# Kernel tuning notes

Measured on AMD Instinct MI355X. Metric: run time of the kernel, lower is better.

The kernel has to match this reference:

```python
import jax, jax.numpy as jnp
import numpy as np

N_NODES = 50000
N_EDGES = 800000
IN_CH = 256
HID = 256
NUM_GRAPHS = 512
LEAKY_SLOPE = 0.01
EPS = 1e-5


def gcn_conv(x, src, dst, W, b):
    # src/dst already include self loops. Symmetric normalization D^-1/2 A_hat D^-1/2.
    deg = jnp.zeros((N_NODES,), x.dtype).at[dst].add(1.0)
    dinv = jax.lax.rsqrt(deg)  # deg >= 1 because of self loops
    norm = dinv[src] * dinv[dst]  # [E+N]
    h = x @ W  # [N, H] dense GEMM
    agg = jnp.zeros((N_NODES, W.shape[1]), x.dtype).at[dst].add(h[src] * norm[:, None])
    return agg + b


def layer_norm(x, w, b):
    mu = jnp.mean(x, axis=-1, keepdims=True)
    var = jnp.mean(jnp.square(x - mu), axis=-1, keepdims=True)
    return (x - mu) * jax.lax.rsqrt(var + EPS) * w + b


def setup_inputs() -> dict:
    key = jax.random.key(0)
    ks = jax.random.split(key, 8)
    x = jax.random.normal(ks[0], (N_NODES, IN_CH), dtype=jnp.float32)
    edge_index = jax.random.randint(ks[1], (2, N_EDGES), 0, N_NODES, dtype=jnp.int64)
    batch = jnp.sort(jax.random.randint(ks[2], (N_NODES,), 0, NUM_GRAPHS, dtype=jnp.int64))
    s1 = (2.0 / IN_CH) ** 0.5
    s2 = (2.0 / HID) ** 0.5
    W1 = jax.random.normal(ks[3], (IN_CH, HID), dtype=jnp.float32) * s1
    b1 = jnp.zeros((HID,), jnp.float32)
    W2 = jax.random.normal(ks[4], (HID, HID), dtype=jnp.float32) * s2
    b2 = jnp.zeros((HID,), jnp.float32)
    ln1_w = jnp.ones((HID,), jnp.float32)
    ln1_b = jnp.zeros((HID,), jnp.float32)
    ln2_w = jnp.ones((HID,), jnp.float32)
    ln2_b = jnp.zeros((HID,), jnp.float32)
    return {"x": x, "edge_index": edge_index, "batch": batch,
            "W1": W1, "b1": b1, "ln1_w": ln1_w, "ln1_b": ln1_b,
            "W2": W2, "b2": b2, "ln2_w": ln2_w, "ln2_b": ln2_b}


def reference(x, edge_index, batch, W1, b1, ln1_w, ln1_b, W2, b2, ln2_w, ln2_b):
    loop = jnp.arange(N_NODES, dtype=edge_index.dtype)
    src = jnp.concatenate([edge_index[0], loop])
    dst = jnp.concatenate([edge_index[1], loop])

    h = gcn_conv(x, src, dst, W1, b1)
    h = layer_norm(h, ln1_w, ln1_b)
    h = jnp.where(h >= 0, h, LEAKY_SLOPE * h)

    h = gcn_conv(h, src, dst, W2, b2)
    h = layer_norm(h, ln2_w, ln2_b)
    h = jnp.where(h >= 0, h, LEAKY_SLOPE * h)

    # global mean pool per graph (dropout is inference no-op)
    sums = jax.ops.segment_sum(h, batch, num_segments=NUM_GRAPHS)
    cnts = jax.ops.segment_sum(jnp.ones((N_NODES,), h.dtype), batch, num_segments=NUM_GRAPHS)
    return sums / jnp.maximum(cnts, 1.0)[:, None]
```

## Files before the change

kernel.cpp:

```cpp
#include <hip/hip_runtime.h>

#define N_NODES 50000
#define N_EDGES 800000
#define CH 256
#define NUM_GRAPHS 512
#define LEAKY 0.01f
#define LN_EPS 1e-5f
#define NBLK ((N_NODES + 255) / 256)

typedef __attribute__((ext_vector_type(4))) float f32x4;
typedef __attribute__((ext_vector_type(2))) float f32x2;
typedef __attribute__((ext_vector_type(8))) short bf16x8;

__device__ __forceinline__ float b2f(unsigned short u) {
    union { unsigned int i; float f; } x; x.i = ((unsigned int)u) << 16; return x.f;
}
__device__ __forceinline__ unsigned short f2b(float f) {
    union { float f; unsigned int i; } x; x.f = f;
    unsigned int r = x.i + 0x7fffu + ((x.i >> 16) & 1u);
    return (unsigned short)(r >> 16);
}
__device__ __forceinline__ f32x2 b2f2(unsigned int u) {
    union { unsigned int i; float f; } lo, hi;
    lo.i = u << 16; hi.i = u & 0xffff0000u;
    f32x2 r; r.x = lo.f; r.y = hi.f; return r;
}
__device__ __forceinline__ unsigned int pack2(float a, float b) {
    return (unsigned int)f2b(a) | ((unsigned int)f2b(b) << 16);
}
__device__ __forceinline__ void gload16(const void* g, void* l) {
    __builtin_amdgcn_global_load_lds((const __attribute__((address_space(1))) unsigned int*)g,
                                     (__attribute__((address_space(3))) unsigned int*)l, 16, 0, 0);
}

__global__ void zero_ints(int* __restrict__ p, int n) {
    int i = blockIdx.x * blockDim.x + threadIdx.x;
    if (i < n) p[i] = 0;
}

__global__ void count_deg(const int* __restrict__ dst, int* __restrict__ cnt) {
    int e = blockIdx.x * blockDim.x + threadIdx.x;
    if (e < N_EDGES) atomicAdd(&cnt[dst[e]], 1);
}

__global__ __launch_bounds__(256) void block_reduce(const int* __restrict__ cnt,
                                                    int* __restrict__ bsum,
                                                    float* __restrict__ dinv) {
    __shared__ int s[256];
    int tid = threadIdx.x;
    int i = blockIdx.x * 256 + tid;
    int v = (i < N_NODES) ? cnt[i] : 0;
    if (i < N_NODES) dinv[i] = rsqrtf(1.0f + (float)v);
    s[tid] = v;
    __syncthreads();
    #pragma unroll
    for (int off = 128; off > 0; off >>= 1) {
        if (tid < off) s[tid] += s[tid + off];
        __syncthreads();
    }
    if (tid == 0) bsum[blockIdx.x] = s[0];
}

__global__ __launch_bounds__(256) void scan_bsums(int* __restrict__ bsum) {
    __shared__ int s[256];
    int tid = threadIdx.x;
    int v = (tid < NBLK) ? bsum[tid] : 0;
    s[tid] = v;
    __syncthreads();
    #pragma unroll
    for (int off = 1; off < 256; off <<= 1) {
        int t = (tid >= off) ? s[tid - off] : 0;
        __syncthreads();
        s[tid] += t;
        __syncthreads();
    }
    if (tid < NBLK) bsum[tid] = s[tid] - v;
}

__global__ __launch_bounds__(256) void block_scan(const int* __restrict__ cnt,
                                                  const int* __restrict__ bsum,
                                                  int* __restrict__ rowptr,
                                                  int* __restrict__ cursor) {
    __shared__ int s[256];
    int tid = threadIdx.x;
    int i = blockIdx.x * 256 + tid;
    int v = (i < N_NODES) ? cnt[i] : 0;
    s[tid] = v;
    __syncthreads();
    #pragma unroll
    for (int off = 1; off < 256; off <<= 1) {
        int t = (tid >= off) ? s[tid - off] : 0;
        __syncthreads();
        s[tid] += t;
        __syncthreads();
    }
    if (i < N_NODES) {
        int val = bsum[blockIdx.x] + s[tid] - v;
        rowptr[i] = val;
        cursor[i] = val;
        if (i == N_NODES - 1) rowptr[N_NODES] = bsum[blockIdx.x] + s[tid];
    }
}

__global__ void fill_csr(const int* __restrict__ src, const int* __restrict__ dst,
                         int* __restrict__ cursor, int* __restrict__ col) {
    int e = blockIdx.x * blockDim.x + threadIdx.x;
    if (e < N_EDGES) {
        int d = dst[e];
        int p = atomicAdd(&cursor[d], 1);
        col[p] = src[e];
    }
}

__global__ void transpose_w2(const float* __restrict__ W1f, const float* __restrict__ W2f,
                             unsigned short* __restrict__ WT1, unsigned short* __restrict__ WT2) {
    int k = blockIdx.x & 255;
    const float* W = (blockIdx.x >> 8) ? W2f : W1f;
    unsigned short* WT = (blockIdx.x >> 8) ? WT2 : WT1;
    int n = threadIdx.x;
    WT[n * CH + k] = f2b(W[k * CH + n]);
}

#define BM 128
#define BN 128
#define BK 64
#define SWZ(row, kb) (((row) * 128 + (kb) * 16) ^ (((row) & 7) << 4))

__global__ __launch_bounds__(256) void gemm_bf16(const unsigned short* __restrict__ A,
                                                 const unsigned short* __restrict__ BT,
                                                 const float* __restrict__ dinv,
                                                 unsigned short* __restrict__ out) {
    __shared__ unsigned short As[BM * BK];
    __shared__ unsigned short Bs[BN * BK];
    const int row0 = blockIdx.x * BM;
    const int col0 = blockIdx.y * BN;
    const int tid = threadIdx.x;
    const int w = tid >> 6, l = tid & 63;
    const int wr = w >> 1, wc = w & 1;
    const int lr = l & 15, lg = l >> 4;

    const int sr = l >> 3;
    const int kbp = l & 7;

    f32x4 acc[4][4] = {};

    for (int k0 = 0; k0 < CH; k0 += BK) {
        #pragma unroll
        for (int it = 0; it < 4; it++) {
            const int R = (w * 4 + it) * 8;
            const int r = R + sr;
            const int kb = kbp ^ (r & 7);
            gload16(&A[(size_t)(row0 + r) * CH + k0 + kb * 8], (char*)As + R * 128);
            gload16(&BT[(size_t)(col0 + r) * CH + k0 + kb * 8], (char*)Bs + R * 128);
        }
        __syncthreads();
        #pragma unroll
        for (int ks = 0; ks < 2; ks++) {
            bf16x8 af[4], bfr[4];
            #pragma unroll
            for (int fm = 0; fm < 4; fm++) {
                int r = wr * 64 + fm * 16 + lr;
                af[fm] = *(const bf16x8*)((const char*)As + SWZ(r, ks * 4 + lg));
            }
            #pragma unroll
            for (int fn = 0; fn < 4; fn++) {
                int r = wc * 64 + fn * 16 + lr;
                bfr[fn] = *(const bf16x8*)((const char*)Bs + SWZ(r, ks * 4 + lg));
            }
            #pragma unroll
            for (int fm = 0; fm < 4; fm++)
                #pragma unroll
                for (int fn = 0; fn < 4; fn++)
                    acc[fm][fn] = __builtin_amdgcn_mfma_f32_16x16x32_bf16(af[fm], bfr[fn], acc[fm][fn], 0, 0, 0);
        }
        __syncthreads();
    }
    #pragma unroll
    for (int fm = 0; fm < 4; fm++) {
        #pragma unroll
        for (int r = 0; r < 4; r++) {
            int grow = row0 + wr * 64 + fm * 16 + lg * 4 + r;
            if (grow < N_NODES) {
                float s = dinv[grow];
                #pragma unroll
                for (int fn = 0; fn < 4; fn++) {
                    int gcol = col0 + wc * 64 + fn * 16 + lr;
                    out[(size_t)grow * CH + gcol] = f2b(acc[fm][fn][r] * s);
                }
            }
        }
    }
}

__global__ __launch_bounds__(256) void gemm_f32a(const float* __restrict__ Af,
                                                 const unsigned short* __restrict__ BT,
                                                 const float* __restrict__ dinv,
                                                 unsigned short* __restrict__ out) {
    __shared__ unsigned short As[BM * BK];
    __shared__ unsigned short Bs[BN * BK];
    const int row0 = blockIdx.x * BM;
    const int col0 = blockIdx.y * BN;
    const int tid = threadIdx.x;
    const int w = tid >> 6, l = tid & 63;
    const int wr = w >> 1, wc = w & 1;
    const int lr = l & 15, lg = l >> 4;
    const int sr = l >> 3, kbp = l & 7;

    f32x4 acc[4][4] = {};

    for (int k0 = 0; k0 < CH; k0 += BK) {
        #pragma unroll
        for (int it = 0; it < 4; it++) {
            const int R = (w * 4 + it) * 8;
            const int r = R + sr;
            const int kb = kbp ^ (r & 7);
            gload16(&BT[(size_t)(col0 + r) * CH + k0 + kb * 8], (char*)Bs + R * 128);
        }
        #pragma unroll
        for (int it = 0; it < 4; it++) {
            int cidx = it * 256 + tid;
            int r = cidx >> 3, kb = cidx & 7;
            int grow = row0 + r;
            uint4 ua = make_uint4(0u, 0u, 0u, 0u);
            if (grow < N_NODES) {
                const float* ap = &Af[(size_t)grow * CH + k0 + kb * 8];
                float4 v0 = *(const float4*)ap;
                float4 v1 = *(const float4*)(ap + 4);
                ua = make_uint4(pack2(v0.x, v0.y), pack2(v0.z, v0.w),
                                pack2(v1.x, v1.y), pack2(v1.z, v1.w));
            }
            *(uint4*)((char*)As + SWZ(r, kb)) = ua;
        }
        __syncthreads();
        #pragma unroll
        for (int ks = 0; ks < 2; ks++) {
            bf16x8 af[4], bfr[4];
            #pragma unroll
            for (int fm = 0; fm < 4; fm++) {
                int r = wr * 64 + fm * 16 + lr;
                af[fm] = *(const bf16x8*)((const char*)As + SWZ(r, ks * 4 + lg));
            }
            #pragma unroll
            for (int fn = 0; fn < 4; fn++) {
                int r = wc * 64 + fn * 16 + lr;
                bfr[fn] = *(const bf16x8*)((const char*)Bs + SWZ(r, ks * 4 + lg));
            }
            #pragma unroll
            for (int fm = 0; fm < 4; fm++)
                #pragma unroll
                for (int fn = 0; fn < 4; fn++)
                    acc[fm][fn] = __builtin_amdgcn_mfma_f32_16x16x32_bf16(af[fm], bfr[fn], acc[fm][fn], 0, 0, 0);
        }
        __syncthreads();
    }
    #pragma unroll
    for (int fm = 0; fm < 4; fm++) {
        #pragma unroll
        for (int r = 0; r < 4; r++) {
            int grow = row0 + wr * 64 + fm * 16 + lg * 4 + r;
            if (grow < N_NODES) {
                float s = dinv[grow];
                #pragma unroll
                for (int fn = 0; fn < 4; fn++) {
                    int gcol = col0 + wc * 64 + fn * 16 + lr;
                    out[(size_t)grow * CH + gcol] = f2b(acc[fm][fn][r] * s);
                }
            }
        }
    }
}

__global__ __launch_bounds__(256) void agg_ln_bf16(const unsigned short* __restrict__ h,
                                                   const int* __restrict__ rowptr,
                                                   const int* __restrict__ col,
                                                   const float* __restrict__ dinv,
                                                   const float* __restrict__ bias,
                                                   const float* __restrict__ lnw,
                                                   const float* __restrict__ lnb,
                                                   unsigned short* __restrict__ out) {
    const int w = threadIdx.x >> 6, lane = threadIdx.x & 63;
    const int d = blockIdx.x * 4 + w;
    if (d >= N_NODES) return;
    const int c4 = lane * 4;
    const uint2* __restrict__ h2 = (const uint2*)h;

    f32x2 acc01, acc23;
    {
        uint2 u = h2[(unsigned)(d * 64 + lane)];
        acc01 = b2f2(u.x); acc23 = b2f2(u.y);
    }

    const int e0 = rowptr[d], e1 = rowptr[d + 1];
    for (int base = e0; base < e1; base += 64) {
        int nch = e1 - base; if (nch > 64) nch = 64;
        int cidx = (lane < nch) ? col[base + lane] : 0;
        int j = 0;
        for (; j + 8 <= nch; j += 8) {
            int s0 = __shfl(cidx, j),     s1 = __shfl(cidx, j + 1);
            int s2 = __shfl(cidx, j + 2), s3 = __shfl(cidx, j + 3);
            int s4 = __shfl(cidx, j + 4), s5 = __shfl(cidx, j + 5);
            int s6 = __shfl(cidx, j + 6), s7 = __shfl(cidx, j + 7);
            uint2 u0 = h2[(unsigned)(s0 * 64 + lane)];
            uint2 u1 = h2[(unsigned)(s1 * 64 + lane)];
            uint2 u2 = h2[(unsigned)(s2 * 64 + lane)];
            uint2 u3 = h2[(unsigned)(s3 * 64 + lane)];
            uint2 u4 = h2[(unsigned)(s4 * 64 + lane)];
            uint2 u5 = h2[(unsigned)(s5 * 64 + lane)];
            uint2 u6 = h2[(unsigned)(s6 * 64 + lane)];
            uint2 u7 = h2[(unsigned)(s7 * 64 + lane)];
            acc01 += b2f2(u0.x) + b2f2(u1.x) + b2f2(u2.x) + b2f2(u3.x);
            acc23 += b2f2(u0.y) + b2f2(u1.y) + b2f2(u2.y) + b2f2(u3.y);
            acc01 += b2f2(u4.x) + b2f2(u5.x) + b2f2(u6.x) + b2f2(u7.x);
            acc23 += b2f2(u4.y) + b2f2(u5.y) + b2f2(u6.y) + b2f2(u7.y);
        }
        for (; j + 4 <= nch; j += 4) {
            int s0 = __shfl(cidx, j),     s1 = __shfl(cidx, j + 1);
            int s2 = __shfl(cidx, j + 2), s3 = __shfl(cidx, j + 3);
            uint2 u0 = h2[(unsigned)(s0 * 64 + lane)];
            uint2 u1 = h2[(unsigned)(s1 * 64 + lane)];
            uint2 u2 = h2[(unsigned)(s2 * 64 + lane)];
            uint2 u3 = h2[(unsigned)(s3 * 64 + lane)];
            acc01 += b2f2(u0.x) + b2f2(u1.x) + b2f2(u2.x) + b2f2(u3.x);
            acc23 += b2f2(u0.y) + b2f2(u1.y) + b2f2(u2.y) + b2f2(u3.y);
        }
        for (; j < nch; j++) {
            int s = __shfl(cidx, j);
            uint2 u = h2[(unsigned)(s * 64 + lane)];
            acc01 += b2f2(u.x); acc23 += b2f2(u.y);
        }
    }
    float a0 = acc01.x, a1 = acc01.y, a2 = acc23.x, a3 = acc23.y;
    const float di = dinv[d];
    float4 bb = *(const float4*)&bias[c4];
    a0 = a0 * di + bb.x; a1 = a1 * di + bb.y; a2 = a2 * di + bb.z; a3 = a3 * di + bb.w;

    float s1 = a0 + a1 + a2 + a3;
    float s2 = a0 * a0 + a1 * a1 + a2 * a2 + a3 * a3;
    #pragma unroll
    for (int off = 32; off > 0; off >>= 1) {
        s1 += __shfl_xor(s1, off);
        s2 += __shfl_xor(s2, off);
    }
    const float mu = s1 * (1.0f / CH);
    const float rstd = rsqrtf(s2 * (1.0f / CH) - mu * mu + LN_EPS);
    float4 wv = *(const float4*)&lnw[c4];
    float4 bv = *(const float4*)&lnb[c4];
    float y0 = (a0 - mu) * rstd * wv.x + bv.x;
    float y1 = (a1 - mu) * rstd * wv.y + bv.y;
    float y2 = (a2 - mu) * rstd * wv.z + bv.z;
    float y3 = (a3 - mu) * rstd * wv.w + bv.w;
    y0 = (y0 >= 0.f) ? y0 : LEAKY * y0;
    y1 = (y1 >= 0.f) ? y1 : LEAKY * y1;
    y2 = (y2 >= 0.f) ? y2 : LEAKY * y2;
    y3 = (y3 >= 0.f) ? y3 : LEAKY * y3;
    *(ushort4*)&out[(size_t)d * CH + c4] = make_ushort4(f2b(y0), f2b(y1), f2b(y2), f2b(y3));
}

__global__ __launch_bounds__(256) void pool_mean_bf16(const unsigned short* __restrict__ feat,
                                                      const int* __restrict__ batch,
                                                      float* __restrict__ out) {
    const int g = blockIdx.x;
    const int w = threadIdx.x >> 6, lane = threadIdx.x & 63;
    int lo = 0, hi = N_NODES;
    while (lo < hi) { int mid = (lo + hi) >> 1; if (batch[mid] < g) lo = mid + 1; else hi = mid; }
    const int start = lo;
    hi = N_NODES;
    while (lo < hi) { int mid = (lo + hi) >> 1; if (batch[mid] < g + 1) lo = mid + 1; else hi = mid; }
    const int end = lo;

    float a0 = 0.f, a1 = 0.f, a2 = 0.f, a3 = 0.f;
    for (int n = start + w; n < end; n += 4) {
        ushort4 u = *(const ushort4*)&feat[(size_t)n * CH + lane * 4];
        a0 += b2f(u.x); a1 += b2f(u.y); a2 += b2f(u.z); a3 += b2f(u.w);
    }
    __shared__ float4 red[4][64];
    red[w][lane] = make_float4(a0, a1, a2, a3);
    __syncthreads();
    if (w == 0) {
        float4 t0 = red[0][lane], t1 = red[1][lane], t2 = red[2][lane], t3 = red[3][lane];
        const float inv = (end > start) ? 1.0f / (float)(end - start) : 0.0f;
        float4 o = make_float4((t0.x + t1.x + t2.x + t3.x) * inv,
                               (t0.y + t1.y + t2.y + t3.y) * inv,
                               (t0.z + t1.z + t2.z + t3.z) * inv,
                               (t0.w + t1.w + t2.w + t3.w) * inv);
        *(float4*)&out[(size_t)g * CH + lane * 4] = o;
    }
}

static inline size_t align256(size_t x) { return (x + 255) & ~(size_t)255; }

extern "C" void kernel_launch(void* const* d_in, const int* in_sizes, int n_in,
                              void* d_out, int out_size, void* d_ws, size_t ws_size,
                              hipStream_t stream) {
    const float* x    = (const float*)d_in[0];
    const int*   edge = (const int*)d_in[1];
    const int*   batch= (const int*)d_in[2];
    const float* W1   = (const float*)d_in[3];
    const float* b1   = (const float*)d_in[4];
    const float* ln1w = (const float*)d_in[5];
    const float* ln1b = (const float*)d_in[6];
    const float* W2   = (const float*)d_in[7];
    const float* b2   = (const float*)d_in[8];
    const float* ln2w = (const float*)d_in[9];
    const float* ln2b = (const float*)d_in[10];

    const int* src = edge;
    const int* dst = edge + N_EDGES;

    char* p = (char*)d_ws;
    int* cnt    = (int*)p;  p += align256(N_NODES * 4);
    int* cursor = (int*)p;  p += align256(N_NODES * 4);
    int* rowptr = (int*)p;  p += align256((N_NODES + 1) * 4);
    int* bsum   = (int*)p;  p += align256(NBLK * 4);
    float* dinv = (float*)p; p += align256(N_NODES * 4);
    int* col    = (int*)p;  p += align256(N_EDGES * 4);
    unsigned short* wt1 = (unsigned short*)p; p += align256(CH * CH * 2);
    unsigned short* wt2 = (unsigned short*)p; p += align256(CH * CH * 2);
    unsigned short* bufA = (unsigned short*)p; p += align256((size_t)N_NODES * CH * 2);
    unsigned short* bufB = (unsigned short*)p; p += align256((size_t)N_NODES * CH * 2);
    p += 32768;

    zero_ints<<<(N_NODES + 255) / 256, 256, 0, stream>>>(cnt, N_NODES);
    count_deg<<<(N_EDGES + 255) / 256, 256, 0, stream>>>(dst, cnt);
    block_reduce<<<NBLK, 256, 0, stream>>>(cnt, bsum, dinv);
    scan_bsums<<<1, 256, 0, stream>>>(bsum);
    block_scan<<<NBLK, 256, 0, stream>>>(cnt, bsum, rowptr, cursor);
    fill_csr<<<(N_EDGES + 255) / 256, 256, 0, stream>>>(src, dst, cursor, col);
    transpose_w2<<<2 * CH, CH, 0, stream>>>(W1, W2, wt1, wt2);

    dim3 ggrid((N_NODES + BM - 1) / BM, CH / BN);
    gemm_f32a<<<ggrid, 256, 0, stream>>>(x, wt1, dinv, bufA);
    agg_ln_bf16<<<(N_NODES + 3) / 4, 256, 0, stream>>>(bufA, rowptr, col, dinv, b1, ln1w, ln1b, bufB);
    gemm_bf16<<<ggrid, 256, 0, stream>>>(bufB, wt2, dinv, bufA);
    agg_ln_bf16<<<(N_NODES + 3) / 4, 256, 0, stream>>>(bufA, rowptr, col, dinv, b2, ln2w, ln2b, bufB);
    pool_mean_bf16<<<NUM_GRAPHS, 256, 0, stream>>>(bufB, batch, (float*)d_out);
}
```

Measured before the change: 293.0 us.

## Widen GEMM tiles to full width and fuse small setup kernels

Each GEMM block now covers all 256 output columns (BN=256) instead of 128, so every A tile is loaded into LDS only once. This cuts A-side global traffic and halves the grid, at the cost of twice the accumulator registers and more LDS per block, which may lower occupancy. The count-zeroing and weight-transpose kernels are merged into one launch, and the block-sum scan is folded into block_scan so each block redoes it redundantly. LeakyReLU becomes a single fmaxf.

```diff
diff --git a/kernel.cpp b/kernel.cpp
--- a/kernel.cpp
+++ b/kernel.cpp
@@ -33,9 +33,20 @@
                                      (__attribute__((address_space(3))) unsigned int*)l, 16, 0, 0);
 }
 
-__global__ void zero_ints(int* __restrict__ p, int n) {
-    int i = blockIdx.x * blockDim.x + threadIdx.x;
-    if (i < n) p[i] = 0;
+__global__ void prep(int* __restrict__ cnt,
+                     const float* __restrict__ W1f, const float* __restrict__ W2f,
+                     unsigned short* __restrict__ WT1, unsigned short* __restrict__ WT2) {
+    int b = blockIdx.x;
+    if (b < NBLK) {
+        int i = b * 256 + threadIdx.x;
+        if (i < N_NODES) cnt[i] = 0;
+    } else {
+        int bb = b - NBLK;
+        int k = bb & 255;
+        const float* W = (bb >> 8) ? W2f : W1f;
+        unsigned short* WT = (bb >> 8) ? WT2 : WT1;
+        WT[threadIdx.x * CH + k] = f2b(W[k * CH + threadIdx.x]);
+    }
 }
 
 __global__ void count_deg(const int* __restrict__ dst, int* __restrict__ cnt) {
@@ -61,29 +72,24 @@
     if (tid == 0) bsum[blockIdx.x] = s[0];
 }
 
-__global__ __launch_bounds__(256) void scan_bsums(int* __restrict__ bsum) {
-    __shared__ int s[256];
-    int tid = threadIdx.x;
-    int v = (tid < NBLK) ? bsum[tid] : 0;
-    s[tid] = v;
-    __syncthreads();
-    #pragma unroll
-    for (int off = 1; off < 256; off <<= 1) {
-        int t = (tid >= off) ? s[tid - off] : 0;
-        __syncthreads();
-        s[tid] += t;
-        __syncthreads();
-    }
-    if (tid < NBLK) bsum[tid] = s[tid] - v;
-}
-
 __global__ __launch_bounds__(256) void block_scan(const int* __restrict__ cnt,
                                                   const int* __restrict__ bsum,
                                                   int* __restrict__ rowptr,
                                                   int* __restrict__ cursor) {
-    __shared__ int s[256];
+    __shared__ int s[256], sb[256];
     int tid = threadIdx.x;
     int i = blockIdx.x * 256 + tid;
+    int bv = (tid < NBLK) ? bsum[tid] : 0;
+    sb[tid] = bv;
+    __syncthreads();
+    #pragma unroll
+    for (int off = 1; off < 256; off <<= 1) {
+        int t = (tid >= off) ? sb[tid - off] : 0;
+        __syncthreads();
+        sb[tid] += t;
+        __syncthreads();
+    }
+    const int base = (blockIdx.x == 0) ? 0 : sb[blockIdx.x - 1];
     int v = (i < N_NODES) ? cnt[i] : 0;
     s[tid] = v;
     __syncthreads();
@@ -95,10 +101,10 @@
         __syncthreads();
     }
     if (i < N_NODES) {
-        int val = bsum[blockIdx.x] + s[tid] - v;
+        int val = base + s[tid] - v;
         rowptr[i] = val;
         cursor[i] = val;
-        if (i == N_NODES - 1) rowptr[N_NODES] = bsum[blockIdx.x] + s[tid];
+        if (i == N_NODES - 1) rowptr[N_NODES] = base + s[tid];
     }
 }
 
@@ -112,17 +118,8 @@
     }
 }
 
-__global__ void transpose_w2(const float* __restrict__ W1f, const float* __restrict__ W2f,
-                             unsigned short* __restrict__ WT1, unsigned short* __restrict__ WT2) {
-    int k = blockIdx.x & 255;
-    const float* W = (blockIdx.x >> 8) ? W2f : W1f;
-    unsigned short* WT = (blockIdx.x >> 8) ? WT2 : WT1;
-    int n = threadIdx.x;
-    WT[n * CH + k] = f2b(W[k * CH + n]);
-}
-
 #define BM 128
-#define BN 128
+#define BN 256
 #define BK 64
 #define SWZ(row, kb) (((row) * 128 + (kb) * 16) ^ (((row) & 7) << 4))
 
@@ -133,16 +130,13 @@
     __shared__ unsigned short As[BM * BK];
     __shared__ unsigned short Bs[BN * BK];
     const int row0 = blockIdx.x * BM;
-    const int col0 = blockIdx.y * BN;
     const int tid = threadIdx.x;
     const int w = tid >> 6, l = tid & 63;
     const int wr = w >> 1, wc = w & 1;
     const int lr = l & 15, lg = l >> 4;
-
-    const int sr = l >> 3;
-    const int kbp = l & 7;
-
-    f32x4 acc[4][4] = {};
+    const int sr = l >> 3, kbp = l & 7;
+
+    f32x4 acc[4][8] = {};
 
     for (int k0 = 0; k0 < CH; k0 += BK) {
         #pragma unroll
@@ -151,26 +145,32 @@
             const int r = R + sr;
             const int kb = kbp ^ (r & 7);
             gload16(&A[(size_t)(row0 + r) * CH + k0 + kb * 8], (char*)As + R * 128);
-            gload16(&BT[(size_t)(col0 + r) * CH + k0 + kb * 8], (char*)Bs + R * 128);
+        }
+        #pragma unroll
+        for (int it = 0; it < 8; it++) {
+            const int R = w * 64 + it * 8;
+            const int r = R + sr;
+            const int kb = kbp ^ (r & 7);
+            gload16(&BT[(size_t)r * CH + k0 + kb * 8], (char*)Bs + R * 128);
         }
         __syncthreads();
         #pragma unroll
         for (int ks = 0; ks < 2; ks++) {
-            bf16x8 af[4], bfr[4];
+            bf16x8 af[4], bfr[8];
             #pragma unroll
             for (int fm = 0; fm < 4; fm++) {
                 int r = wr * 64 + fm * 16 + lr;
                 af[fm] = *(const bf16x8*)((const char*)As + SWZ(r, ks * 4 + lg));
             }
             #pragma unroll
-            for (int fn = 0; fn < 4; fn++) {
-                int r = wc * 64 + fn * 16 + lr;
+            for (int fn = 0; fn < 8; fn++) {
+                int r = wc * 128 + fn * 16 + lr;
                 bfr[fn] = *(const bf16x8*)((const char*)Bs + SWZ(r, ks * 4 + lg));
             }
             #pragma unroll
             for (int fm = 0; fm < 4; fm++)
                 #pragma unroll
-                for (int fn = 0; fn < 4; fn++)
+                for (int fn = 0; fn < 8; fn++)
                     acc[fm][fn] = __builtin_amdgcn_mfma_f32_16x16x32_bf16(af[fm], bfr[fn], acc[fm][fn], 0, 0, 0);
         }
         __syncthreads();
@@ -183,8 +183,8 @@
             if (grow < N_NODES) {
                 float s = dinv[grow];
                 #pragma unroll
-                for (int fn = 0; fn < 4; fn++) {
-                    int gcol = col0 + wc * 64 + fn * 16 + lr;
+                for (int fn = 0; fn < 8; fn++) {
+                    int gcol = wc * 128 + fn * 16 + lr;
                     out[(size_t)grow * CH + gcol] = f2b(acc[fm][fn][r] * s);
                 }
             }
@@ -199,22 +199,21 @@
     __shared__ unsigned short As[BM * BK];
     __shared__ unsigned short Bs[BN * BK];
     const int row0 = blockIdx.x * BM;
-    const int col0 = blockIdx.y * BN;
     const int tid = threadIdx.x;
     const int w = tid >> 6, l = tid & 63;
     const int wr = w >> 1, wc = w & 1;
     const int lr = l & 15, lg = l >> 4;
     const int sr = l >> 3, kbp = l & 7;
 
-    f32x4 acc[4][4] = {};
+    f32x4 acc[4][8] = {};
 
     for (int k0 = 0; k0 < CH; k0 += BK) {
         #pragma unroll
-        for (int it = 0; it < 4; it++) {
-            const int R = (w * 4 + it) * 8;
+        for (int it = 0; it < 8; it++) {
+            const int R = w * 64 + it * 8;
             const int r = R + sr;
             const int kb = kbp ^ (r & 7);
-            gload16(&BT[(size_t)(col0 + r) * CH + k0 + kb * 8], (char*)Bs + R * 128);
+            gload16(&BT[(size_t)r * CH + k0 + kb * 8], (char*)Bs + R * 128);
         }
         #pragma unroll
         for (int it = 0; it < 4; it++) {
@@ -234,21 +233,21 @@
         __syncthreads();
         #pragma unroll
         for (int ks = 0; ks < 2; ks++) {
-            bf16x8 af[4], bfr[4];
+            bf16x8 af[4], bfr[8];
             #pragma unroll
             for (int fm = 0; fm < 4; fm++) {
                 int r = wr * 64 + fm * 16 + lr;
                 af[fm] = *(const bf16x8*)((const char*)As + SWZ(r, ks * 4 + lg));
             }
             #pragma unroll
-            for (int fn = 0; fn < 4; fn++) {
-                int r = wc * 64 + fn * 16 + lr;
+            for (int fn = 0; fn < 8; fn++) {
+                int r = wc * 128 + fn * 16 + lr;
                 bfr[fn] = *(const bf16x8*)((const char*)Bs + SWZ(r, ks * 4 + lg));
             }
             #pragma unroll
             for (int fm = 0; fm < 4; fm++)
                 #pragma unroll
-                for (int fn = 0; fn < 4; fn++)
+                for (int fn = 0; fn < 8; fn++)
                     acc[fm][fn] = __builtin_amdgcn_mfma_f32_16x16x32_bf16(af[fm], bfr[fn], acc[fm][fn], 0, 0, 0);
         }
         __syncthreads();
@@ -261,8 +260,8 @@
             if (grow < N_NODES) {
                 float s = dinv[grow];
                 #pragma unroll
-                for (int fn = 0; fn < 4; fn++) {
-                    int gcol = col0 + wc * 64 + fn * 16 + lr;
+                for (int fn = 0; fn < 8; fn++) {
+                    int gcol = wc * 128 + fn * 16 + lr;
                     out[(size_t)grow * CH + gcol] = f2b(acc[fm][fn][r] * s);
                 }
             }
@@ -349,10 +348,10 @@
     float y1 = (a1 - mu) * rstd * wv.y + bv.y;
     float y2 = (a2 - mu) * rstd * wv.z + bv.z;
     float y3 = (a3 - mu) * rstd * wv.w + bv.w;
-    y0 = (y0 >= 0.f) ? y0 : LEAKY * y0;
-    y1 = (y1 >= 0.f) ? y1 : LEAKY * y1;
-    y2 = (y2 >= 0.f) ? y2 : LEAKY * y2;
-    y3 = (y3 >= 0.f) ? y3 : LEAKY * y3;
+    y0 = fmaxf(y0, LEAKY * y0);
+    y1 = fmaxf(y1, LEAKY * y1);
+    y2 = fmaxf(y2, LEAKY * y2);
+    y3 = fmaxf(y3, LEAKY * y3);
     *(ushort4*)&out[(size_t)d * CH + c4] = make_ushort4(f2b(y0), f2b(y1), f2b(y2), f2b(y3));
 }
 
@@ -420,15 +419,13 @@
     unsigned short* bufB = (unsigned short*)p; p += align256((size_t)N_NODES * CH * 2);
     p += 32768;
 
-    zero_ints<<<(N_NODES + 255) / 256, 256, 0, stream>>>(cnt, N_NODES);
+    prep<<<NBLK + 2 * CH, 256, 0, stream>>>(cnt, W1, W2, wt1, wt2);
     count_deg<<<(N_EDGES + 255) / 256, 256, 0, stream>>>(dst, cnt);
     block_reduce<<<NBLK, 256, 0, stream>>>(cnt, bsum, dinv);
-    scan_bsums<<<1, 256, 0, stream>>>(bsum);
     block_scan<<<NBLK, 256, 0, stream>>>(cnt, bsum, rowptr, cursor);
     fill_csr<<<(N_EDGES + 255) / 256, 256, 0, stream>>>(src, dst, cursor, col);
-    transpose_w2<<<2 * CH, CH, 0, stream>>>(W1, W2, wt1, wt2);
-
-    dim3 ggrid((N_NODES + BM - 1) / BM, CH / BN);
+
+    const int ggrid = (N_NODES + BM - 1) / BM;
     gemm_f32a<<<ggrid, 256, 0, stream>>>(x, wt1, dinv, bufA);
     agg_ln_bf16<<<(N_NODES + 3) / 4, 256, 0, stream>>>(bufA, rowptr, col, dinv, b1, ln1w, ln1b, bufB);
     gemm_bf16<<<ggrid, 256, 0, stream>>>(bufB, wt2, dinv, bufA);
```

Result: no change. 296.9 us (+1.3%).
